# Kernel optimization log

Hardware: AMD Instinct MI355X
Metric: run time of the kernel (lower is better)

Reference implementation:

```python
import jax, jax.numpy as jnp
import numpy as np

B, S, D, H = 16, 512, 1024, 16
DH = D // H  # 64


def setup_inputs() -> dict:
    key = jax.random.key(0)
    kx, kq, kk, kv = jax.random.split(key, 4)
    stdv = 1.0 / np.sqrt(DH)  # reset_param uses 1/sqrt(t.size(1)) = 1/sqrt(head_dim)
    x = jax.random.normal(kx, (B, S, D), dtype=jnp.float32)
    Wq = jax.random.uniform(kq, (H, D, DH), dtype=jnp.float32, minval=-stdv, maxval=stdv)
    Wk = jax.random.uniform(kk, (H, D, DH), dtype=jnp.float32, minval=-stdv, maxval=stdv)
    Wv = jax.random.uniform(kv, (H, D, DH), dtype=jnp.float32, minval=-stdv, maxval=stdv)
    return {"x": x, "Wq": Wq, "Wk": Wk, "Wv": Wv}


def reference(x, Wq, Wk, Wv):
    # x: [B, S, D]; Wq/Wk/Wv: [H, D, DH] (stacked per-head params)
    q = jnp.einsum('bsd,hde->bhse', x, Wq)  # [B,H,S,DH]
    k = jnp.einsum('bsd,hde->bhse', x, Wk)
    v = jnp.einsum('bsd,hde->bhse', x, Wv)
    # NOTE: original scales by sqrt(input_dim), not sqrt(head_dim)
    scale = 1.0 / jnp.sqrt(jnp.float32(D))
    scores = jnp.einsum('bhse,bhte->bhst', q, k) * scale  # [B,H,S,S]
    attn = jax.nn.softmax(scores, axis=-1)
    out = jnp.einsum('bhst,bhte->bhse', attn, v)  # [B,H,S,DH]
    # concat heads along feature dim (head order matches torch cat over loop)
    return out.transpose(0, 2, 1, 3).reshape(x.shape[0], x.shape[1], D)
```

## Files before the change

### kernel.cpp

```cpp
#include <hip/hip_runtime.h>
#include <math.h>

constexpr int B = 16, S = 512, D = 1024, H = 16, DH = 64;
constexpr int BH = B * H;

typedef short bf16x8 __attribute__((ext_vector_type(8)));
typedef float f32x4  __attribute__((ext_vector_type(4)));

__device__ __forceinline__ unsigned short f2bf(float f) {
    unsigned u = __float_as_uint(f);
    u += 0x7fff + ((u >> 16) & 1);
    return (unsigned short)(u >> 16);
}

#define VMC0  asm volatile("s_waitcnt vmcnt(0)" ::: "memory")
#define LGKM0 asm volatile("s_waitcnt lgkmcnt(0)" ::: "memory")
#define BARR  __builtin_amdgcn_s_barrier()

__global__ __launch_bounds__(256) void convert_all(
    const float* __restrict__ x, unsigned short* __restrict__ xb,
    const float* __restrict__ Wq, const float* __restrict__ Wk,
    const float* __restrict__ Wv, unsigned short* __restrict__ WbT)
{
    __shared__ float tile[64][65];
    const int t = threadIdx.x;
    const int bx = blockIdx.x;

    if (bx < 8192) {
        int i = bx * 256 + t;
        float4 v = ((const float4*)x)[i];
        ushort4 o;
        o.x = f2bf(v.x); o.y = f2bf(v.y); o.z = f2bf(v.z); o.w = f2bf(v.w);
        ((ushort4*)xb)[i] = o;
        return;
    }

    const int cw = bx - 8192;
    const int d0 = (cw & 15) * 64;
    const int h = (cw >> 4) & 15;
    const int m = cw >> 8;
    const float* W = ((m == 0) ? Wq : (m == 1) ? Wk : Wv) + (size_t)h * D * DH;
    {
        int e = t & 63, dr = t >> 6;
        #pragma unroll
        for (int i = 0; i < 16; ++i) {
            int d = dr * 16 + i;
            tile[d][e] = W[(size_t)(d0 + d) * DH + e];
        }
    }
    __syncthreads();
    {
        int d = t & 63, er = t >> 6;
        unsigned short* out = WbT + (size_t)(m * H + h) * DH * D;
        #pragma unroll
        for (int i = 0; i < 16; ++i) {
            int e = er * 16 + i;
            out[(size_t)e * D + d0 + d] = f2bf(tile[d][e]);
        }
    }
}

__device__ __forceinline__ void qkv_stage(
    const unsigned short* __restrict__ xb,
    const unsigned short* __restrict__ WbT,
    unsigned short* Ad, unsigned short* Bd,
    int r0, int n0, int k0, int w, int lrow8, int lg)
{
    #pragma unroll
    for (int i = 0; i < 4; ++i) {
        int c = w * 4 + i;
        int r = c * 8 + lrow8;
        int gg = lg ^ (r & 7);
        __builtin_amdgcn_global_load_lds(
            (const __attribute__((address_space(1))) void*)
                (xb + (size_t)(r0 + r) * D + k0 + gg * 8),
            (__attribute__((address_space(3))) void*)(Ad + c * 512),
            16, 0, 0);
        __builtin_amdgcn_global_load_lds(
            (const __attribute__((address_space(1))) void*)
                (WbT + (size_t)(n0 + r) * D + k0 + gg * 8),
            (__attribute__((address_space(3))) void*)(Bd + c * 512),
            16, 0, 0);
    }
}

__global__ __launch_bounds__(256) void qkv_gemm(
    const unsigned short* __restrict__ xb,
    const unsigned short* __restrict__ WbT,
    unsigned short* __restrict__ qkvb)
{
    __shared__ unsigned short As[2][128 * 64];
    __shared__ unsigned short Bs[2][128 * 64];

    const int t = threadIdx.x;
    const int w = t >> 6;
    const int wr = w >> 1, wc = w & 1;
    const int L = t & 63;
    const int lane15 = L & 15;
    const int quad = L >> 4;
    const int lrow8 = L >> 3;
    const int lg = L & 7;

    const int r0 = blockIdx.x * 128;
    const int n0 = blockIdx.y * 128;

    f32x4 acc[4][4] = {};

    qkv_stage(xb, WbT, &As[0][0], &Bs[0][0], r0, n0, 0, w, lrow8, lg);
    VMC0;
    BARR;

    #pragma unroll 2
    for (int kt = 0; kt < 16; ++kt) {
        const int cur = kt & 1;

        bf16x8 a[2][4], bb[2][4];
        #pragma unroll
        for (int ks = 0; ks < 2; ++ks) {
            int gk = ks * 4 + quad;
            #pragma unroll
            for (int rt = 0; rt < 4; ++rt) {
                int ml = wr * 64 + rt * 16 + lane15;
                a[ks][rt] = *(const bf16x8*)(&As[cur][0] + ml * 64 + ((gk ^ (ml & 7)) * 8));
            }
            #pragma unroll
            for (int ct = 0; ct < 4; ++ct) {
                int nl = wc * 64 + ct * 16 + lane15;
                bb[ks][ct] = *(const bf16x8*)(&Bs[cur][0] + nl * 64 + ((gk ^ (nl & 7)) * 8));
            }
        }
        __builtin_amdgcn_sched_barrier(0);

        if (kt < 15)
            qkv_stage(xb, WbT, &As[cur ^ 1][0], &Bs[cur ^ 1][0],
                      r0, n0, (kt + 1) * 64, w, lrow8, lg);

        __builtin_amdgcn_s_setprio(1);
        #pragma unroll
        for (int ks = 0; ks < 2; ++ks)
            #pragma unroll
            for (int rt = 0; rt < 4; ++rt)
                #pragma unroll
                for (int ct = 0; ct < 4; ++ct)
                    acc[rt][ct] = __builtin_amdgcn_mfma_f32_16x16x32_bf16(
                        a[ks][rt], bb[ks][ct], acc[rt][ct], 0, 0, 0);
        __builtin_amdgcn_s_setprio(0);

        VMC0;
        BARR;
    }

    const int m  = n0 >> 10;
    const int h  = ((n0 >> 6) + wc) & 15;
    const int bb_ = r0 >> 9;
    const int s0 = (r0 & 511) + wr * 64;

    if (m == 2) {
        unsigned short* outv = qkvb + ((size_t)(2 * BH) + (bb_ * H + h)) * (size_t)(S * DH);
        #pragma unroll
        for (int rt = 0; rt < 4; ++rt) {
            int srow = s0 + rt * 16 + quad * 4;
            #pragma unroll
            for (int ct = 0; ct < 4; ++ct) {
                int e = ct * 16 + lane15;
                ushort4 pk;
                pk.x = f2bf(acc[rt][ct][0]);
                pk.y = f2bf(acc[rt][ct][1]);
                pk.z = f2bf(acc[rt][ct][2]);
                pk.w = f2bf(acc[rt][ct][3]);
                *(ushort4*)(outv + (size_t)e * S + srow) = pk;
            }
        }
    } else {
        const float sc = (m == 0) ? 0.04508422002778011f : 1.0f;
        unsigned short* out = qkvb + ((size_t)m * BH + (bb_ * H + h)) * (size_t)(S * DH);
        #pragma unroll
        for (int rt = 0; rt < 4; ++rt) {
            #pragma unroll
            for (int ct = 0; ct < 4; ++ct) {
                int e = ct * 16 + lane15;
                #pragma unroll
                for (int r = 0; r < 4; ++r) {
                    int srow = s0 + rt * 16 + quad * 4 + r;
                    out[(size_t)srow * DH + e] = f2bf(acc[rt][ct][r] * sc);
                }
            }
        }
    }
}

__device__ __forceinline__ void stage_kv(
    const unsigned short* __restrict__ kb, const unsigned short* __restrict__ vt,
    int kt, unsigned short* Kd, unsigned short* Vd, int w, int lrow8, int lg)
{
    #pragma unroll
    for (int i = 0; i < 2; ++i) {
        int base = (w * 2 + i) * 8;
        int r = base + lrow8;
        int gr = (r & 32) | ((r & 12) << 1) | ((r & 16) >> 2) | (r & 3);
        int gg = lg ^ (r & 7);
        __builtin_amdgcn_global_load_lds(
            (const __attribute__((address_space(1))) void*)
                (kb + (size_t)(kt + gr) * DH + gg * 8),
            (__attribute__((address_space(3))) void*)(Kd + base * 64),
            16, 0, 0);
        __builtin_amdgcn_global_load_lds(
            (const __attribute__((address_space(1))) void*)
                (vt + (size_t)r * S + kt + gg * 8),
            (__attribute__((address_space(3))) void*)(Vd + base * 64),
            16, 0, 0);
    }
}

__global__ __launch_bounds__(256) void attn_mfma(
    const unsigned short* __restrict__ qkvb, float* __restrict__ out)
{
    __shared__ unsigned short KV[2][2][64 * 64];
    unsigned short* Qs = &KV[0][0][0];

    const int t = threadIdx.x;
    const int w = t >> 6;
    const int L = t & 63;
    const int lane15 = L & 15;
    const int quad = L >> 4;
    const int lrow8 = L >> 3;
    const int lg = L & 7;
    const int qr0 = blockIdx.x * 256;
    const int bh = blockIdx.y;
    const int b = bh >> 4, h = bh & 15;

    const unsigned short* qb = qkvb + (size_t)bh * S * DH;
    const unsigned short* kb = qkvb + (size_t)(BH + bh) * S * DH;
    const unsigned short* vt = qkvb + (size_t)(2 * BH + bh) * S * DH;

    #pragma unroll
    for (int i = 0; i < 8; ++i) {
        int base = i * 32 + w * 8;
        int r = base + lrow8;
        int gg = lg ^ (r & 7);
        __builtin_amdgcn_global_load_lds(
            (const __attribute__((address_space(1))) void*)
                (qb + (size_t)(qr0 + r) * DH + gg * 8),
            (__attribute__((address_space(3))) void*)(Qs + base * 64),
            16, 0, 0);
    }
    VMC0;
    BARR;

    bf16x8 qf[4][2];
    #pragma unroll
    for (int mt = 0; mt < 4; ++mt)
        #pragma unroll
        for (int ks = 0; ks < 2; ++ks) {
            int ml = w * 64 + mt * 16 + lane15;
            int gk = ks * 4 + quad;
            qf[mt][ks] = *(const bf16x8*)(Qs + ml * 64 + ((gk ^ (lane15 & 7)) * 8));
        }
    LGKM0;
    BARR;

    stage_kv(kb, vt, 0, &KV[0][0][0], &KV[0][1][0], w, lrow8, lg);
    VMC0;
    BARR;

    f32x4 o[4][4] = {};
    float plsum[4] = {0.f, 0.f, 0.f, 0.f};

    #pragma unroll 2
    for (int kt = 0; kt < 8; ++kt) {
        const int cur = kt & 1;

        bf16x8 kf[2][4], vf[2][4];
        #pragma unroll
        for (int ks = 0; ks < 2; ++ks) {
            int gk = ks * 4 + quad;
            #pragma unroll
            for (int ct = 0; ct < 4; ++ct) {
                int kr = ct * 16 + lane15;
                kf[ks][ct] = *(const bf16x8*)(&KV[cur][0][0] + kr * 64 + ((gk ^ (lane15 & 7)) * 8));
                vf[ks][ct] = *(const bf16x8*)(&KV[cur][1][0] + kr * 64 + ((gk ^ (lane15 & 7)) * 8));
            }
        }
        __builtin_amdgcn_sched_barrier(0);

        if (kt < 7)
            stage_kv(kb, vt, (kt + 1) * 64, &KV[cur ^ 1][0][0], &KV[cur ^ 1][1][0],
                     w, lrow8, lg);

        f32x4 st[4][4] = {};
        __builtin_amdgcn_s_setprio(1);
        #pragma unroll
        for (int ks = 0; ks < 2; ++ks)
            #pragma unroll
            for (int mt = 0; mt < 4; ++mt)
                #pragma unroll
                for (int ct = 0; ct < 4; ++ct)
                    st[mt][ct] = __builtin_amdgcn_mfma_f32_16x16x32_bf16(
                        kf[ks][ct], qf[mt][ks], st[mt][ct], 0, 0, 0);
        __builtin_amdgcn_s_setprio(0);

        bf16x8 pB[4][2];
        #pragma unroll
        for (int mt = 0; mt < 4; ++mt) {
            float rs = 0.f;
            union { unsigned u[4]; bf16x8 v; } pu[2];
            #pragma unroll
            for (int ct = 0; ct < 4; ++ct) {
                float p0 = exp2f(st[mt][ct][0]);
                float p1 = exp2f(st[mt][ct][1]);
                float p2 = exp2f(st[mt][ct][2]);
                float p3 = exp2f(st[mt][ct][3]);
                rs += (p0 + p1) + (p2 + p3);
                unsigned lo, hi;
                asm("v_cvt_pk_bf16_f32 %0, %1, %2" : "=v"(lo) : "v"(p0), "v"(p1));
                asm("v_cvt_pk_bf16_f32 %0, %1, %2" : "=v"(hi) : "v"(p2), "v"(p3));
                pu[ct >> 1].u[(ct & 1) * 2 + 0] = lo;
                pu[ct >> 1].u[(ct & 1) * 2 + 1] = hi;
            }
            pB[mt][0] = pu[0].v;
            pB[mt][1] = pu[1].v;
            plsum[mt] += rs;
        }

        __builtin_amdgcn_s_setprio(1);
        #pragma unroll
        for (int ks = 0; ks < 2; ++ks)
            #pragma unroll
            for (int mt = 0; mt < 4; ++mt)
                #pragma unroll
                for (int nt = 0; nt < 4; ++nt)
                    o[mt][nt] = __builtin_amdgcn_mfma_f32_16x16x32_bf16(
                        vf[ks][nt], pB[mt][ks], o[mt][nt], 0, 0, 0);
        __builtin_amdgcn_s_setprio(0);

        VMC0;
        BARR;
    }

    #pragma unroll
    for (int mt = 0; mt < 4; ++mt) {
        float l = plsum[mt];
        l += __shfl_xor(l, 16, 64);
        l += __shfl_xor(l, 32, 64);
        float inv = 1.0f / l;
        int srow = qr0 + w * 64 + mt * 16 + lane15;
        float* op = out + (size_t)(b * S + srow) * D + h * DH;
        #pragma unroll
        for (int nt = 0; nt < 4; ++nt) {
            float4 v;
            v.x = o[mt][nt][0] * inv;
            v.y = o[mt][nt][1] * inv;
            v.z = o[mt][nt][2] * inv;
            v.w = o[mt][nt][3] * inv;
            *(float4*)(op + nt * 16 + quad * 4) = v;
        }
    }
}

extern "C" void kernel_launch(void* const* d_in, const int* in_sizes, int n_in,
                              void* d_out, int out_size, void* d_ws, size_t ws_size,
                              hipStream_t stream) {
    const float* x  = (const float*)d_in[0];
    const float* Wq = (const float*)d_in[1];
    const float* Wk = (const float*)d_in[2];
    const float* Wv = (const float*)d_in[3];
    float* outp = (float*)d_out;

    unsigned short* qkvb = (unsigned short*)d_ws;
    unsigned short* xb   = (unsigned short*)((char*)d_ws + 50331648);
    unsigned short* WbT  = (unsigned short*)((char*)d_ws + 67108864);

    convert_all<<<dim3(8192 + 768), 256, 0, stream>>>(x, xb, Wq, Wk, Wv, WbT);
    qkv_gemm<<<dim3(B * S / 128, 3 * H * DH / 128), 256, 0, stream>>>(xb, WbT, qkvb);
    attn_mfma<<<dim3(S / 256, BH), 256, 0, stream>>>(qkvb, outp);
}
```

Before: 189.0 us.

## Shrink attention query tile to 128 rows and swizzle QKV GEMM block order

```diff
diff --git a/kernel.cpp b/kernel.cpp
--- a/kernel.cpp
+++ b/kernel.cpp
@@ -101,8 +101,10 @@
     const int lrow8 = L >> 3;
     const int lg = L & 7;
 
-    const int r0 = blockIdx.x * 128;
-    const int n0 = blockIdx.y * 128;
+    const int flat = blockIdx.y * 64 + blockIdx.x;
+    const int swz  = (flat & 7) * 192 + (flat >> 3);
+    const int r0 = (swz & 63) * 128;
+    const int n0 = (swz >> 6) * 128;
 
     f32x4 acc[4][4] = {};
 
@@ -215,8 +217,9 @@
 __global__ __launch_bounds__(256) void attn_mfma(
     const unsigned short* __restrict__ qkvb, float* __restrict__ out)
 {
-    __shared__ unsigned short KV[2][2][64 * 64];
-    unsigned short* Qs = &KV[0][0][0];
+    __shared__ unsigned short Qs[128 * 64];
+    __shared__ unsigned short Ks[2][64 * 64];
+    __shared__ unsigned short Vt[2][64 * 64];
 
     const int t = threadIdx.x;
     const int w = t >> 6;
@@ -225,7 +228,7 @@
     const int quad = L >> 4;
     const int lrow8 = L >> 3;
     const int lg = L & 7;
-    const int qr0 = blockIdx.x * 256;
+    const int qr0 = blockIdx.x * 128;
     const int bh = blockIdx.y;
     const int b = bh >> 4, h = bh & 15;
 
@@ -234,41 +237,37 @@
     const unsigned short* vt = qkvb + (size_t)(2 * BH + bh) * S * DH;
 
     #pragma unroll
-    for (int i = 0; i < 8; ++i) {
-        int base = i * 32 + w * 8;
+    for (int i = 0; i < 4; ++i) {
+        int base = w * 32 + i * 8;
         int r = base + lrow8;
         int gg = lg ^ (r & 7);
-        __builtin_amdgcn_global_load_lds(
-            (const __attribute__((address_space(1))) void*)
-                (qb + (size_t)(qr0 + r) * DH + gg * 8),
+        const unsigned short* gp = qb + (size_t)(qr0 + r) * DH + gg * 8;
+        __builtin_amdgcn_global_load_lds(
+            (const __attribute__((address_space(1))) void*)gp,
             (__attribute__((address_space(3))) void*)(Qs + base * 64),
             16, 0, 0);
     }
+    stage_kv(kb, vt, 0, &Ks[0][0], &Vt[0][0], w, lrow8, lg);
     VMC0;
     BARR;
 
-    bf16x8 qf[4][2];
-    #pragma unroll
-    for (int mt = 0; mt < 4; ++mt)
+    bf16x8 qf[2][2];
+    #pragma unroll
+    for (int mt = 0; mt < 2; ++mt)
         #pragma unroll
         for (int ks = 0; ks < 2; ++ks) {
-            int ml = w * 64 + mt * 16 + lane15;
+            int ml = w * 32 + mt * 16 + lane15;
             int gk = ks * 4 + quad;
             qf[mt][ks] = *(const bf16x8*)(Qs + ml * 64 + ((gk ^ (lane15 & 7)) * 8));
         }
-    LGKM0;
-    BARR;
-
-    stage_kv(kb, vt, 0, &KV[0][0][0], &KV[0][1][0], w, lrow8, lg);
-    VMC0;
-    BARR;
-
-    f32x4 o[4][4] = {};
-    float plsum[4] = {0.f, 0.f, 0.f, 0.f};
+
+    f32x4 o[2][4] = {};
+    float plsum[2] = {0.f, 0.f};
 
     #pragma unroll 2
-    for (int kt = 0; kt < 8; ++kt) {
-        const int cur = kt & 1;
+    for (int kt = 0; kt < S; kt += 64) {
+        const int cur = (kt >> 6) & 1;
+        const int nxt = cur ^ 1;
 
         bf16x8 kf[2][4], vf[2][4];
         #pragma unroll
@@ -277,31 +276,30 @@
             #pragma unroll
             for (int ct = 0; ct < 4; ++ct) {
                 int kr = ct * 16 + lane15;
-                kf[ks][ct] = *(const bf16x8*)(&KV[cur][0][0] + kr * 64 + ((gk ^ (lane15 & 7)) * 8));
-                vf[ks][ct] = *(const bf16x8*)(&KV[cur][1][0] + kr * 64 + ((gk ^ (lane15 & 7)) * 8));
+                kf[ks][ct] = *(const bf16x8*)(&Ks[cur][0] + kr * 64 + ((gk ^ (lane15 & 7)) * 8));
+                vf[ks][ct] = *(const bf16x8*)(&Vt[cur][0] + kr * 64 + ((gk ^ (lane15 & 7)) * 8));
             }
         }
         __builtin_amdgcn_sched_barrier(0);
 
-        if (kt < 7)
-            stage_kv(kb, vt, (kt + 1) * 64, &KV[cur ^ 1][0][0], &KV[cur ^ 1][1][0],
-                     w, lrow8, lg);
-
-        f32x4 st[4][4] = {};
+        if (kt + 64 < S)
+            stage_kv(kb, vt, kt + 64, &Ks[nxt][0], &Vt[nxt][0], w, lrow8, lg);
+
+        f32x4 st[2][4] = {};
         __builtin_amdgcn_s_setprio(1);
         #pragma unroll
         for (int ks = 0; ks < 2; ++ks)
             #pragma unroll
-            for (int mt = 0; mt < 4; ++mt)
+            for (int mt = 0; mt < 2; ++mt)
                 #pragma unroll
                 for (int ct = 0; ct < 4; ++ct)
                     st[mt][ct] = __builtin_amdgcn_mfma_f32_16x16x32_bf16(
                         kf[ks][ct], qf[mt][ks], st[mt][ct], 0, 0, 0);
         __builtin_amdgcn_s_setprio(0);
 
-        bf16x8 pB[4][2];
-        #pragma unroll
-        for (int mt = 0; mt < 4; ++mt) {
+        bf16x8 pB[2][2];
+        #pragma unroll
+        for (int mt = 0; mt < 2; ++mt) {
             float rs = 0.f;
             union { unsigned u[4]; bf16x8 v; } pu[2];
             #pragma unroll
@@ -326,7 +324,7 @@
         #pragma unroll
         for (int ks = 0; ks < 2; ++ks)
             #pragma unroll
-            for (int mt = 0; mt < 4; ++mt)
+            for (int mt = 0; mt < 2; ++mt)
                 #pragma unroll
                 for (int nt = 0; nt < 4; ++nt)
                     o[mt][nt] = __builtin_amdgcn_mfma_f32_16x16x32_bf16(
@@ -338,12 +336,12 @@
     }
 
     #pragma unroll
-    for (int mt = 0; mt < 4; ++mt) {
+    for (int mt = 0; mt < 2; ++mt) {
         float l = plsum[mt];
         l += __shfl_xor(l, 16, 64);
         l += __shfl_xor(l, 32, 64);
         float inv = 1.0f / l;
-        int srow = qr0 + w * 64 + mt * 16 + lane15;
+        int srow = qr0 + w * 32 + mt * 16 + lane15;
         float* op = out + (size_t)(b * S + srow) * D + h * DH;
         #pragma unroll
         for (int nt = 0; nt < 4; ++nt) {
@@ -372,5 +370,5 @@
 
     convert_all<<<dim3(8192 + 768), 256, 0, stream>>>(x, xb, Wq, Wk, Wv, WbT);
     qkv_gemm<<<dim3(B * S / 128, 3 * H * DH / 128), 256, 0, stream>>>(xb, WbT, qkvb);
-    attn_mfma<<<dim3(S / 256, BH), 256, 0, stream>>>(qkvb, outp);
-}
+    attn_mfma<<<dim3(S / 128, BH), 256, 0, stream>>>(qkvb, outp);
+}
```

Result: slower. 201.0 us (+6.4%).
